# Performance work log

Hardware: AMD Instinct MI355X
Metric: run time of the kernel (lower is better)

## Reference

```python
import jax, jax.numpy as jnp
import numpy as np

B, S, D, L = 128, 256, 256, 3          # graphs, nodes/graph (=max_set_size), feat dim, gnn layers
E = 524288                              # edges per graph-set (avg degree 16)
N = B * S                               # total nodes per side
TAU, N_SINK, EPS_GIN, BN_EPS = 0.1, 20, 1.0, 1e-5


def setup_inputs() -> dict:
    key = jax.random.key(0)
    ks = jax.random.split(key, 16)
    sc = 1.0 / np.sqrt(D)
    inp = {
        "features_1": jax.random.normal(ks[0], (N, D), jnp.float32),
        "features_2": jax.random.normal(ks[1], (N, D), jnp.float32),
        "edge_index_1": jax.random.randint(ks[2], (2, E), 0, N),
        "edge_index_2": jax.random.randint(ks[3], (2, E), 0, N),
        "u_noise": jax.random.uniform(ks[4], (B, S, S), jnp.float32),
        # stacked GIN MLP params (3 identical-shape layers)
        "gin_w1": jax.random.normal(ks[5], (L, D, D), jnp.float32) * sc,
        "gin_b1": jnp.zeros((L, D), jnp.float32),
        "gin_w2": jax.random.normal(ks[6], (L, D, D), jnp.float32) * sc,
        "gin_b2": jnp.zeros((L, D), jnp.float32),
        "gin_gamma": jnp.ones((L, D), jnp.float32),
        "gin_beta": jnp.zeros((L, D), jnp.float32),
        # fc_transform1/2 and bilinear W
        "fc1_w": jax.random.normal(ks[7], (D, D), jnp.float32) * sc,
        "fc1_b": jnp.zeros((D,), jnp.float32),
        "fc2_w": jax.random.normal(ks[8], (D, D), jnp.float32) * sc,
        "fc2_b": jnp.zeros((D,), jnp.float32),
        "W": jax.random.normal(ks[9], (D, D), jnp.float32) * sc,
    }
    return inp


def _forward(features_1, features_2, u_noise, gin_w1, gin_b1, gin_w2, gin_b2,
             gin_gamma, gin_beta, fc1_w, fc1_b, fc2_w, fc2_b, W,
             edge_index_1, edge_index_2):
    def gin_stack(x, ei):
        src, dst = ei[0], ei[1]
        for l in range(L):
            # GINConv: nn((1+eps)*x + sum_{j->i} x_j), eps=True -> 1.0
            aggr = jax.ops.segment_sum(x[src], dst, num_segments=N)
            h = (1.0 + EPS_GIN) * x + aggr
            h = jax.nn.relu(h @ gin_w1[l] + gin_b1[l])
            h = h @ gin_w2[l] + gin_b2[l]
            mu = jnp.mean(h, axis=0)
            var = jnp.var(h, axis=0)                      # BatchNorm1d, training stats
            h = gin_gamma[l] * (h - mu) * jax.lax.rsqrt(var + BN_EPS) + gin_beta[l]
            x = jax.nn.relu(h)                            # outer relu (dropout p=0)
        return x

    g1 = gin_stack(features_1, edge_index_1).reshape(B, S, D)  # all graphs have S nodes -> no pad
    g2 = gin_stack(features_2, edge_index_2).reshape(B, S, D)

    def transform(g):
        return jax.nn.relu(g @ fc1_w + fc1_b) @ fc2_w + fc2_b

    m1 = transform(g1)   # masks are all-ones since every graph is full-size
    m2 = transform(g2)
    scores = jnp.einsum('bsd,de,bte->bst', m1, W, m2)          # [B,S,S]

    gumbel = -jnp.log(-jnp.log(u_noise + 1e-20) + 1e-20)
    log_alpha = (scores + gumbel) / TAU
    for _ in range(N_SINK):
        log_alpha = log_alpha - jax.scipy.special.logsumexp(log_alpha, axis=-1, keepdims=True)
        log_alpha = log_alpha - jax.scipy.special.logsumexp(log_alpha, axis=-2, keepdims=True)
    P = jnp.exp(log_alpha)

    p = jnp.sum(g1 - jnp.matmul(P, g2), axis=(1, 2))           # [B]
    p = (p - p.min()) / (p.max() - p.min())
    return jnp.exp(-p)


def reference(features_1, features_2, edge_index_1, edge_index_2, u_noise,
              gin_w1, gin_b1, gin_w2, gin_b2, gin_gamma, gin_beta,
              fc1_w, fc1_b, fc2_w, fc2_b, W):
    return _forward(features_1, features_2, u_noise, gin_w1, gin_b1, gin_w2, gin_b2,
                    gin_gamma, gin_beta, fc1_w, fc1_b, fc2_w, fc2_b, W,
                    edge_index_1, edge_index_2)
```

## Files before the change

### kernel.cpp

```cpp
#include <hip/hip_runtime.h>


constexpr int NNODE = 32768;
constexpr int NEDGE = 524288;

typedef __attribute__((ext_vector_type(8))) short bf16x8;
typedef __attribute__((ext_vector_type(4))) float f32x4;

__device__ __forceinline__ float bf2f(unsigned short u) {
  return __uint_as_float((unsigned)u << 16);
}
__device__ __forceinline__ unsigned short f2bf(float f) {
  unsigned u = __float_as_uint(f);
  return (unsigned short)((u + 0x7FFFu + ((u >> 16) & 1u)) >> 16);
}
__device__ __forceinline__ unsigned packbf(float a, float b) {
  return (unsigned)f2bf(a) | ((unsigned)f2bf(b) << 16);
}

__global__ __launch_bounds__(256) void k_prep(
    const float* __restrict__ f1, const float* __restrict__ f2,
    unsigned short* __restrict__ hb0,
    const float* __restrict__ gw1, const float* __restrict__ gw2,
    unsigned short* __restrict__ Wt,
    const int* __restrict__ e1, const int* __restrict__ e2,
    int* __restrict__ cnt, unsigned short* __restrict__ srcs64) {
  __shared__ float sh[64][65];
  int b = blockIdx.x, t = threadIdx.x;
  if (b < 16384) {
    size_t i = (size_t)b * 256 + t;
    const float* src = (i < 2097152) ? (f1 + i * 4) : (f2 + (i - 2097152) * 4);
    float4 v = *(const float4*)src;
    ushort4 o;
    o.x = f2bf(v.x); o.y = f2bf(v.y); o.z = f2bf(v.z); o.w = f2bf(v.w);
    *(ushort4*)(hb0 + i * 4) = o;
  } else if (b < 16480) {
    int bb = b - 16384;
    int mat = bb >> 4, tile = bb & 15;
    int tr = (tile >> 2) * 64, tc = (tile & 3) * 64;
    const float* src = (mat < 3) ? (gw1 + (size_t)mat * 65536) : (gw2 + (size_t)(mat - 3) * 65536);
#pragma unroll
    for (int i = 0; i < 4; i++) {
      int c = t + i * 256;
      int row = c >> 4, c4 = (c & 15) * 4;
      float4 v = *(const float4*)(src + (size_t)(tr + row) * 256 + tc + c4);
      sh[row][c4] = v.x; sh[row][c4 + 1] = v.y; sh[row][c4 + 2] = v.z; sh[row][c4 + 3] = v.w;
    }
    __syncthreads();
#pragma unroll
    for (int i = 0; i < 2; i++) {
      int c = t + i * 256;
      int n = c >> 3, kc = (c & 7) * 8;
      unsigned short e[8];
#pragma unroll
      for (int j = 0; j < 8; j++) e[j] = f2bf(sh[kc + j][n]);
      uint4 o;
      o.x = e[0] | ((unsigned)e[1] << 16);
      o.y = e[2] | ((unsigned)e[3] << 16);
      o.z = e[4] | ((unsigned)e[5] << 16);
      o.w = e[6] | ((unsigned)e[7] << 16);
      int kg = tr + kc;
      size_t idx = (size_t)mat * 65536 + (size_t)(kg >> 5) * 8192 + (size_t)(tc + n) * 32 + (kg & 31);
      *(uint4*)(Wt + idx) = o;
    }
  } else {
    int bb = b - 16480;
    int side = bb >> 11;
    int e = (bb & 2047) * 256 + t;
    const int* ei = (side ? e2 : e1);
    int s = ei[e], d = ei[NEDGE + e];
    int slot = atomicAdd(&cnt[side * NNODE + d], 1);
    if (slot < 64)
      srcs64[(((size_t)side * NNODE + d) << 6) + slot] = (unsigned short)s;
  }
}

template <bool BN>
__global__ __launch_bounds__(512, 4) void k_layer(
    const unsigned short* __restrict__ x,
    const int* __restrict__ cnt,
    const unsigned short* __restrict__ srcs64,
    const float* __restrict__ pstats,
    const float* __restrict__ pgamma, const float* __restrict__ pbeta,
    const unsigned short* __restrict__ w1t,
    const unsigned short* __restrict__ w2t,
    const float* __restrict__ b1, const float* __restrict__ b2,
    float* __restrict__ stats,
    unsigned short* __restrict__ hout) {
  __shared__ __align__(16) char smem[81920];
  char* sA = smem;
  char* sA2 = smem;
  char* sW = smem + 65536;
  float2* red = (float2*)(smem + 65536);
  int tid = threadIdx.x;
  int lane = tid & 63, wid = tid >> 6;
  int wm = wid & 1, wn = wid >> 1;
  int q = lane >> 4, r = lane & 15;
  const int swA = (r & 7) << 4;
  const int swW = ((r >> 1) & 3) << 4;
  int b = blockIdx.x;
  int side = b >> 8;
  size_t grow0 = (size_t)side * NNODE + (size_t)(b & 255) * 128;

  auto stageW = [&](const unsigned short* wsrc, int k0) {
    const unsigned short* basep = wsrc + (size_t)(k0 >> 5) * 8192;
#pragma unroll
    for (int it = 0; it < 2; it++) {
      int c = tid + it * 512;
      int row = c >> 2, ch = c & 3;
      float4 v = *(const float4*)(basep + (size_t)c * 8);
      *(float4*)(sW + row * 64 + ((ch * 16) ^ (((row >> 1) & 3) << 4))) = v;
    }
  };

  stageW(w1t, 0);

  {
    int hw = tid >> 5, sub = tid & 31;
    float sc[8], shf[8];
    if (BN) {
      int c0 = sub * 8;
      const float* cs = pstats + side * 512;
      const float invn = 1.f / 32768.f;
#pragma unroll
      for (int j = 0; j < 8; j++) {
        float mu = cs[c0 + j] * invn;
        float var = cs[256 + c0 + j] * invn - mu * mu;
        float s = pgamma[c0 + j] * rsqrtf(var + 1e-5f);
        sc[j] = s; shf[j] = pbeta[c0 + j] - mu * s;
      }
    }
    const uint4* X = (const uint4*)x;
    size_t rbase = (size_t)side * NNODE;
    const int* degs = cnt + side * NNODE;
    const unsigned short* sr = srcs64 + ((size_t)side * NNODE << 6);
    int nbase = (int)(b & 255) * 128;

#pragma unroll 1
    for (int nn = 0; nn < 8; nn++) {
      int lrow = hw * 8 + nn;
      int n = nbase + lrow;
      float a[8];
#pragma unroll
      for (int j = 0; j < 8; j++) a[j] = 0.f;
      auto acc8 = [&](uint4 u, float w) {
        unsigned uu[4] = {u.x, u.y, u.z, u.w};
#pragma unroll
        for (int j = 0; j < 4; j++) {
          float lo = __uint_as_float(uu[j] << 16);
          float hi = __uint_as_float(uu[j] & 0xFFFF0000u);
          if (BN) {
            lo = fmaxf(fmaf(lo, sc[2 * j], shf[2 * j]), 0.f);
            hi = fmaxf(fmaf(hi, sc[2 * j + 1], shf[2 * j + 1]), 0.f);
          }
          a[2 * j] = fmaf(lo, w, a[2 * j]);
          a[2 * j + 1] = fmaf(hi, w, a[2 * j + 1]);
        }
      };
      acc8(X[(rbase + n) * 32 + sub], 2.f);
      int e = n << 6, ee = (n << 6) + degs[n];
      for (; e + 3 < ee; e += 4) {
        int i0 = sr[e], i1 = sr[e + 1], i2 = sr[e + 2], i3 = sr[e + 3];
        uint4 u0 = X[(rbase + i0) * 32 + sub];
        uint4 u1 = X[(rbase + i1) * 32 + sub];
        uint4 u2 = X[(rbase + i2) * 32 + sub];
        uint4 u3 = X[(rbase + i3) * 32 + sub];
        acc8(u0, 1.f); acc8(u1, 1.f); acc8(u2, 1.f); acc8(u3, 1.f);
      }
      for (; e < ee; e++) acc8(X[(rbase + sr[e]) * 32 + sub], 1.f);
      uint4 o;
      o.x = packbf(a[0], a[1]); o.y = packbf(a[2], a[3]);
      o.z = packbf(a[4], a[5]); o.w = packbf(a[6], a[7]);
      *(uint4*)(sA + lrow * 512 + ((sub * 16) ^ ((lrow & 7) << 4))) = o;
    }
  }

  f32x4 acc[4][4];
#pragma unroll
  for (int mi = 0; mi < 4; mi++)
#pragma unroll
    for (int ni = 0; ni < 4; ni++) acc[mi][ni] = (f32x4){0.f, 0.f, 0.f, 0.f};

  __syncthreads();

  for (int k0 = 0; k0 < 256; k0 += 32) {
    bf16x8 af[4], bfr[4];
    int cbA = (k0 * 2 + q * 16) ^ swA;
    int cbW = (q * 16) ^ swW;
#pragma unroll
    for (int mi = 0; mi < 4; mi++)
      af[mi] = *(const bf16x8*)(sA + (wm * 64 + mi * 16 + r) * 512 + cbA);
#pragma unroll
    for (int ni = 0; ni < 4; ni++)
      bfr[ni] = *(const bf16x8*)(sW + (wn * 64 + ni * 16 + r) * 64 + cbW);
#pragma unroll
    for (int mi = 0; mi < 4; mi++)
#pragma unroll
      for (int ni = 0; ni < 4; ni++)
        acc[mi][ni] = __builtin_amdgcn_mfma_f32_16x16x32_bf16(af[mi], bfr[ni], acc[mi][ni], 0, 0, 0);
    __syncthreads();
    if (k0 < 224) {
      stageW(w1t, k0 + 32);
      __syncthreads();
    }
  }

  float b1v[4];
#pragma unroll
  for (int ni = 0; ni < 4; ni++) b1v[ni] = b1[wn * 64 + ni * 16 + r];
#pragma unroll
  for (int mi = 0; mi < 4; mi++)
#pragma unroll
    for (int ni = 0; ni < 4; ni++)
#pragma unroll
      for (int j = 0; j < 4; j++) {
        float o = fmaxf(acc[mi][ni][j] + b1v[ni], 0.f);
        int rowc = wm * 64 + mi * 16 + q * 4 + j;
        int colc = wn * 64 + ni * 16 + r;
        *(unsigned short*)(sA2 + rowc * 512 + ((colc * 2) ^ (((q * 4 + j) & 7) << 4))) = f2bf(o);
      }
#pragma unroll
  for (int mi = 0; mi < 4; mi++)
#pragma unroll
    for (int ni = 0; ni < 4; ni++) acc[mi][ni] = (f32x4){0.f, 0.f, 0.f, 0.f};
  stageW(w2t, 0);
  __syncthreads();

  for (int k0 = 0; k0 < 256; k0 += 32) {
    bf16x8 af[4], bfr[4];
    int cbA = (k0 * 2 + q * 16) ^ swA;
    int cbW = (q * 16) ^ swW;
#pragma unroll
    for (int mi = 0; mi < 4; mi++)
      af[mi] = *(const bf16x8*)(sA2 + (wm * 64 + mi * 16 + r) * 512 + cbA);
#pragma unroll
    for (int ni = 0; ni < 4; ni++)
      bfr[ni] = *(const bf16x8*)(sW + (wn * 64 + ni * 16 + r) * 64 + cbW);
#pragma unroll
    for (int mi = 0; mi < 4; mi++)
#pragma unroll
      for (int ni = 0; ni < 4; ni++)
        acc[mi][ni] = __builtin_amdgcn_mfma_f32_16x16x32_bf16(af[mi], bfr[ni], acc[mi][ni], 0, 0, 0);
    __syncthreads();
    if (k0 < 224) {
      stageW(w2t, k0 + 32);
      __syncthreads();
    }
  }

  float b2v[4];
#pragma unroll
  for (int ni = 0; ni < 4; ni++) b2v[ni] = b2[wn * 64 + ni * 16 + r];
#pragma unroll
  for (int ni = 0; ni < 4; ni++) {
    float ss = 0.f, sq = 0.f;
#pragma unroll
    for (int mi = 0; mi < 4; mi++)
#pragma unroll
      for (int j = 0; j < 4; j++) {
        float o = acc[mi][ni][j] + b2v[ni];
        acc[mi][ni][j] = o;
        ss += o; sq += o * o;
      }
    ss += __shfl_xor(ss, 16, 64); ss += __shfl_xor(ss, 32, 64);
    sq += __shfl_xor(sq, 16, 64); sq += __shfl_xor(sq, 32, 64);
    if (q == 0) {
      float2 w; w.x = ss; w.y = sq;
      red[(wn * 64 + ni * 16 + r) * 2 + wm] = w;
    }
  }
#pragma unroll
  for (int mi = 0; mi < 4; mi++)
#pragma unroll
    for (int ni = 0; ni < 4; ni++)
#pragma unroll
      for (int j = 0; j < 4; j++) {
        int rowc = wm * 64 + mi * 16 + q * 4 + j;
        int colc = wn * 64 + ni * 16 + r;
        *(unsigned short*)(sA2 + rowc * 512 + ((colc * 2) ^ (((q * 4 + j) & 7) << 4))) =
            f2bf(acc[mi][ni][j]);
      }
  __syncthreads();
  float* cs = stats + side * 512;
  if (tid < 256) {
    float2 a = red[tid * 2], c2 = red[tid * 2 + 1];
    atomicAdd(&cs[tid], a.x + c2.x);
    atomicAdd(&cs[256 + tid], a.y + c2.y);
  }
  for (int c = tid; c < 4096; c += 512) {
    int row = c >> 5, cb = (c & 31) * 16;
    float4 v = *(const float4*)(sA2 + row * 512 + (cb ^ ((row & 7) << 4)));
    *(float4*)(hout + (grow0 + row) * 256 + (c & 31) * 8) = v;
  }
}

__global__ __launch_bounds__(256) void k_gsum(
    const unsigned short* __restrict__ h, const float* __restrict__ stats,
    const float* __restrict__ gamma, const float* __restrict__ beta,
    float* __restrict__ sg) {
  int b = blockIdx.x;
  int side = b >> 7, g = b & 127;
  int t = threadIdx.x;
  int c0 = (t & 63) * 4, rg = t >> 6;
  const float* cs = stats + side * 512;
  float sc[4], sh_[4];
#pragma unroll
  for (int j = 0; j < 4; j++) {
    float mu = cs[c0 + j] * (1.f / 32768.f);
    float var = cs[256 + c0 + j] * (1.f / 32768.f) - mu * mu;
    float s = gamma[c0 + j] * rsqrtf(var + 1e-5f);
    sc[j] = s; sh_[j] = beta[c0 + j] - mu * s;
  }
  size_t base = (size_t)side * NNODE + (size_t)g * 256;
  float acc = 0.f;
  for (int k = 0; k < 64; k++) {
    int row = rg + k * 4;
    ushort4 u = *(const ushort4*)(h + (base + row) * 256 + c0);
    acc += fmaxf(fmaf(bf2f(u.x), sc[0], sh_[0]), 0.f);
    acc += fmaxf(fmaf(bf2f(u.y), sc[1], sh_[1]), 0.f);
    acc += fmaxf(fmaf(bf2f(u.z), sc[2], sh_[2]), 0.f);
    acc += fmaxf(fmaf(bf2f(u.w), sc[3], sh_[3]), 0.f);
  }
  __shared__ float red[256];
  red[t] = acc;
  __syncthreads();
  if (t < 64) {
    float s = red[t] + red[t + 64] + red[t + 128] + red[t + 192];
#pragma unroll
    for (int m = 1; m < 64; m <<= 1) s += __shfl_xor(s, m, 64);
    if (t == 0) sg[b] = s;
  }
}

__global__ void k_final(const float* __restrict__ sg1, const float* __restrict__ sg2,
                        float* __restrict__ out) {
  int t = threadIdx.x;
  float a = sg1[t] - sg2[t];
  float b = sg1[t + 64] - sg2[t + 64];
  float mn = fminf(a, b), mx = fmaxf(a, b);
#pragma unroll
  for (int msk = 1; msk < 64; msk <<= 1) {
    mn = fminf(mn, __shfl_xor(mn, msk, 64));
    mx = fmaxf(mx, __shfl_xor(mx, msk, 64));
  }
  float inv = 1.0f / (mx - mn);
  out[t] = __expf(-(a - mn) * inv);
  out[t + 64] = __expf(-(b - mn) * inv);
}

extern "C" void kernel_launch(void* const* d_in, const int* in_sizes, int n_in,
                              void* d_out, int out_size, void* d_ws, size_t ws_size,
                              hipStream_t stream) {
  (void)in_sizes; (void)n_in; (void)out_size; (void)ws_size;
  const float* f1 = (const float*)d_in[0];
  const float* f2 = (const float*)d_in[1];
  const int* e1 = (const int*)d_in[2];
  const int* e2 = (const int*)d_in[3];
  const float* gw1 = (const float*)d_in[5];
  const float* gb1 = (const float*)d_in[6];
  const float* gw2 = (const float*)d_in[7];
  const float* gb2 = (const float*)d_in[8];
  const float* gga = (const float*)d_in[9];
  const float* gbe = (const float*)d_in[10];
  float* out = (float*)d_out;

  char* ws = (char*)d_ws;
  size_t o = 0;
  auto alloc = [&](size_t bytes) { void* p = ws + o; o += (bytes + 255) & ~(size_t)255; return p; };
  unsigned short* hb0 = (unsigned short*)alloc(2ull * NNODE * 256 * 2);
  unsigned short* hb1 = (unsigned short*)alloc(2ull * NNODE * 256 * 2);
  unsigned short* Wt = (unsigned short*)alloc(6ull * 65536 * 2);
  float* stats = (float*)alloc(3 * 1024 * 4);
  float* sg = (float*)alloc(256 * 4);
  int* cnt = (int*)alloc(2 * NNODE * 4);
  unsigned short* srcs64 = (unsigned short*)alloc(2ull * NNODE * 64 * 2);

  (void)hipMemsetAsync(stats, 0, 3 * 1024 * 4, stream);
  (void)hipMemsetAsync(cnt, 0, 2 * NNODE * 4, stream);

  k_prep<<<20576, 256, 0, stream>>>(f1, f2, hb0, gw1, gw2, Wt, e1, e2, cnt, srcs64);

  unsigned short* hb[2] = {hb0, hb1};
  for (int l = 0; l < 3; l++) {
    unsigned short* xin = hb[l & 1];
    unsigned short* hout = hb[1 - (l & 1)];
    if (l == 0)
      k_layer<false><<<512, 512, 0, stream>>>(
          xin, cnt, srcs64, nullptr, nullptr, nullptr,
          Wt + (size_t)l * 65536, Wt + (size_t)(3 + l) * 65536,
          gb1 + l * 256, gb2 + l * 256, stats + l * 1024, hout);
    else
      k_layer<true><<<512, 512, 0, stream>>>(
          xin, cnt, srcs64, stats + (l - 1) * 1024, gga + (l - 1) * 256, gbe + (l - 1) * 256,
          Wt + (size_t)l * 65536, Wt + (size_t)(3 + l) * 65536,
          gb1 + l * 256, gb2 + l * 256, stats + l * 1024, hout);
  }

  k_gsum<<<256, 256, 0, stream>>>(hb1, stats + 2 * 1024, gga + 512, gbe + 512, sg);
  k_final<<<1, 64, 0, stream>>>(sg, sg + 128, out);
}
```

Before: 429.3 us.

## Sort nodes by degree for balanced aggregation and read weights directly from global

```diff
diff --git a/kernel.cpp b/kernel.cpp
--- a/kernel.cpp
+++ b/kernel.cpp
@@ -75,11 +75,34 @@
   }
 }
 
+__global__ __launch_bounds__(128) void k_sortdeg(const int* __restrict__ cnt,
+                                                 unsigned char* __restrict__ perm) {
+  __shared__ int s[128];
+  int g = blockIdx.x;
+  int side = g >> 8, grp = g & 255;
+  int t = threadIdx.x;
+  int deg = cnt[side * NNODE + grp * 128 + t];
+  s[t] = (deg << 8) | t;
+  __syncthreads();
+  for (int k = 2; k <= 128; k <<= 1)
+    for (int j = k >> 1; j > 0; j >>= 1) {
+      int ixj = t ^ j;
+      if (ixj > t) {
+        int a = s[t], b2 = s[ixj];
+        bool up = ((t & k) == 0);
+        if ((a > b2) == up) { s[t] = b2; s[ixj] = a; }
+      }
+      __syncthreads();
+    }
+  perm[(size_t)side * NNODE + grp * 128 + t] = (unsigned char)(s[t] & 255);
+}
+
 template <bool BN>
 __global__ __launch_bounds__(512, 4) void k_layer(
     const unsigned short* __restrict__ x,
     const int* __restrict__ cnt,
     const unsigned short* __restrict__ srcs64,
+    const unsigned char* __restrict__ perm,
     const float* __restrict__ pstats,
     const float* __restrict__ pgamma, const float* __restrict__ pbeta,
     const unsigned short* __restrict__ w1t,
@@ -87,33 +110,18 @@
     const float* __restrict__ b1, const float* __restrict__ b2,
     float* __restrict__ stats,
     unsigned short* __restrict__ hout) {
-  __shared__ __align__(16) char smem[81920];
+  __shared__ __align__(16) char smem[69632];
   char* sA = smem;
   char* sA2 = smem;
-  char* sW = smem + 65536;
   float2* red = (float2*)(smem + 65536);
   int tid = threadIdx.x;
   int lane = tid & 63, wid = tid >> 6;
   int wm = wid & 1, wn = wid >> 1;
   int q = lane >> 4, r = lane & 15;
   const int swA = (r & 7) << 4;
-  const int swW = ((r >> 1) & 3) << 4;
   int b = blockIdx.x;
   int side = b >> 8;
   size_t grow0 = (size_t)side * NNODE + (size_t)(b & 255) * 128;
-
-  auto stageW = [&](const unsigned short* wsrc, int k0) {
-    const unsigned short* basep = wsrc + (size_t)(k0 >> 5) * 8192;
-#pragma unroll
-    for (int it = 0; it < 2; it++) {
-      int c = tid + it * 512;
-      int row = c >> 2, ch = c & 3;
-      float4 v = *(const float4*)(basep + (size_t)c * 8);
-      *(float4*)(sW + row * 64 + ((ch * 16) ^ (((row >> 1) & 3) << 4))) = v;
-    }
-  };
-
-  stageW(w1t, 0);
 
   {
     int hw = tid >> 5, sub = tid & 31;
@@ -134,11 +142,12 @@
     size_t rbase = (size_t)side * NNODE;
     const int* degs = cnt + side * NNODE;
     const unsigned short* sr = srcs64 + ((size_t)side * NNODE << 6);
+    const unsigned char* pg = perm + (size_t)side * NNODE + (size_t)(b & 255) * 128;
     int nbase = (int)(b & 255) * 128;
 
 #pragma unroll 1
     for (int nn = 0; nn < 8; nn++) {
-      int lrow = hw * 8 + nn;
+      int lrow = pg[nn * 16 + hw];
       int n = nbase + lrow;
       float a[8];
 #pragma unroll
@@ -183,27 +192,24 @@
 
   __syncthreads();
 
+#pragma unroll 2
   for (int k0 = 0; k0 < 256; k0 += 32) {
     bf16x8 af[4], bfr[4];
     int cbA = (k0 * 2 + q * 16) ^ swA;
-    int cbW = (q * 16) ^ swW;
+    const unsigned short* wb = w1t + (size_t)(k0 >> 5) * 8192 + q * 8;
+#pragma unroll
+    for (int ni = 0; ni < 4; ni++)
+      bfr[ni] = *(const bf16x8*)(wb + (size_t)(wn * 64 + ni * 16 + r) * 32);
 #pragma unroll
     for (int mi = 0; mi < 4; mi++)
       af[mi] = *(const bf16x8*)(sA + (wm * 64 + mi * 16 + r) * 512 + cbA);
 #pragma unroll
-    for (int ni = 0; ni < 4; ni++)
-      bfr[ni] = *(const bf16x8*)(sW + (wn * 64 + ni * 16 + r) * 64 + cbW);
-#pragma unroll
     for (int mi = 0; mi < 4; mi++)
 #pragma unroll
       for (int ni = 0; ni < 4; ni++)
         acc[mi][ni] = __builtin_amdgcn_mfma_f32_16x16x32_bf16(af[mi], bfr[ni], acc[mi][ni], 0, 0, 0);
-    __syncthreads();
-    if (k0 < 224) {
-      stageW(w1t, k0 + 32);
-      __syncthreads();
-    }
-  }
+  }
+  __syncthreads();
 
   float b1v[4];
 #pragma unroll
@@ -223,30 +229,26 @@
   for (int mi = 0; mi < 4; mi++)
 #pragma unroll
     for (int ni = 0; ni < 4; ni++) acc[mi][ni] = (f32x4){0.f, 0.f, 0.f, 0.f};
-  stageW(w2t, 0);
-  __syncthreads();
-
+  __syncthreads();
+
+#pragma unroll 2
   for (int k0 = 0; k0 < 256; k0 += 32) {
     bf16x8 af[4], bfr[4];
     int cbA = (k0 * 2 + q * 16) ^ swA;
-    int cbW = (q * 16) ^ swW;
+    const unsigned short* wb = w2t + (size_t)(k0 >> 5) * 8192 + q * 8;
+#pragma unroll
+    for (int ni = 0; ni < 4; ni++)
+      bfr[ni] = *(const bf16x8*)(wb + (size_t)(wn * 64 + ni * 16 + r) * 32);
 #pragma unroll
     for (int mi = 0; mi < 4; mi++)
       af[mi] = *(const bf16x8*)(sA2 + (wm * 64 + mi * 16 + r) * 512 + cbA);
 #pragma unroll
-    for (int ni = 0; ni < 4; ni++)
-      bfr[ni] = *(const bf16x8*)(sW + (wn * 64 + ni * 16 + r) * 64 + cbW);
-#pragma unroll
     for (int mi = 0; mi < 4; mi++)
 #pragma unroll
       for (int ni = 0; ni < 4; ni++)
         acc[mi][ni] = __builtin_amdgcn_mfma_f32_16x16x32_bf16(af[mi], bfr[ni], acc[mi][ni], 0, 0, 0);
-    __syncthreads();
-    if (k0 < 224) {
-      stageW(w2t, k0 + 32);
-      __syncthreads();
-    }
-  }
+  }
+  __syncthreads();
 
   float b2v[4];
 #pragma unroll
@@ -374,11 +376,13 @@
   float* sg = (float*)alloc(256 * 4);
   int* cnt = (int*)alloc(2 * NNODE * 4);
   unsigned short* srcs64 = (unsigned short*)alloc(2ull * NNODE * 64 * 2);
+  unsigned char* perm = (unsigned char*)alloc(2ull * NNODE);
 
   (void)hipMemsetAsync(stats, 0, 3 * 1024 * 4, stream);
   (void)hipMemsetAsync(cnt, 0, 2 * NNODE * 4, stream);
 
   k_prep<<<20576, 256, 0, stream>>>(f1, f2, hb0, gw1, gw2, Wt, e1, e2, cnt, srcs64);
+  k_sortdeg<<<512, 128, 0, stream>>>(cnt, perm);
 
   unsigned short* hb[2] = {hb0, hb1};
   for (int l = 0; l < 3; l++) {
@@ -386,12 +390,12 @@
     unsigned short* hout = hb[1 - (l & 1)];
     if (l == 0)
       k_layer<false><<<512, 512, 0, stream>>>(
-          xin, cnt, srcs64, nullptr, nullptr, nullptr,
+          xin, cnt, srcs64, perm, nullptr, nullptr, nullptr,
           Wt + (size_t)l * 65536, Wt + (size_t)(3 + l) * 65536,
           gb1 + l * 256, gb2 + l * 256, stats + l * 1024, hout);
     else
       k_layer<true><<<512, 512, 0, stream>>>(
-          xin, cnt, srcs64, stats + (l - 1) * 1024, gga + (l - 1) * 256, gbe + (l - 1) * 256,
+          xin, cnt, srcs64, perm, stats + (l - 1) * 1024, gga + (l - 1) * 256, gbe + (l - 1) * 256,
           Wt + (size_t)l * 65536, Wt + (size_t)(3 + l) * 65536,
           gb1 + l * 256, gb2 + l * 256, stats + l * 1024, hout);
   }
```

Result: no change. 422.2 us (-1.7%).
